# Performance work log

Measured on AMD Instinct MI355X. Metric: run time of the kernel, lower is better.

The kernel has to match this reference:

```python
import jax, jax.numpy as jnp
import numpy as np

N_NODES = 50000
N_EDGES = 400000
F_IN = 70
E_DIM = 4
HID = 128
HEADS = 4


def _add_self_loops(src, dst, edge_attr, n):
    # PyG GATConv(add_self_loops=True, fill_value='mean' when edge_dim is set):
    # self-loop edge_attr = per-dst-node mean of incoming edge_attr.
    cnt = jax.ops.segment_sum(jnp.ones((src.shape[0],), edge_attr.dtype), dst, n)
    loop_attr = jax.ops.segment_sum(edge_attr, dst, n) / jnp.clip(cnt, 1.0)[:, None]
    loop = jnp.arange(n, dtype=src.dtype)
    return (jnp.concatenate([src, loop]), jnp.concatenate([dst, loop]),
            jnp.concatenate([edge_attr, loop_attr], axis=0))


def _gat_layer(x, src, dst, e_attr, W, a_src, a_dst, We, a_edge, b, concat):
    # W: [in, H*D]; a_src/a_dst/a_edge: [H, D]; We: [edge_dim, H*D]
    n = x.shape[0]
    H, D = a_src.shape
    xs = (x @ W).reshape(n, H, D)                      # [N,H,D]
    s_src = jnp.einsum('nhd,hd->nh', xs, a_src)        # [N,H]
    s_dst = jnp.einsum('nhd,hd->nh', xs, a_dst)
    ee = (e_attr @ We).reshape(-1, H, D)               # [E,H,D]
    s_edge = jnp.einsum('ehd,hd->eh', ee, a_edge)
    alpha = jax.nn.leaky_relu(s_src[src] + s_dst[dst] + s_edge, 0.2)  # [E,H]
    # segment softmax over edges grouped by destination node
    m = jax.ops.segment_max(alpha, dst, n)
    m = jnp.where(jnp.isfinite(m), m, 0.0)
    ex = jnp.exp(alpha - m[dst])
    denom = jax.ops.segment_sum(ex, dst, n)
    alpha = ex / (denom[dst] + 1e-16)
    msg = xs[src] * alpha[..., None]                   # [E,H,D] -- dominant traffic
    agg = jax.ops.segment_sum(msg, dst, n)             # [N,H,D]
    out = agg.reshape(n, H * D) if concat else agg.mean(axis=1)
    return out + b


def _layer_norm(x, g, b, eps=1e-5):
    mu = x.mean(-1, keepdims=True)
    var = ((x - mu) ** 2).mean(-1, keepdims=True)
    return (x - mu) * jax.lax.rsqrt(var + eps) * g + b


def setup_inputs() -> dict:
    key = jax.random.key(0)
    ks = jax.random.split(key, 24)
    f32 = jnp.float32
    node_features = jax.random.normal(ks[0], (N_NODES, F_IN), f32)
    edge_index = jax.random.randint(ks[1], (2, N_EDGES), 0, N_NODES, jnp.int32)
    edge_attr = jax.random.uniform(ks[2], (N_EDGES, E_DIM), f32)
    s = 0.1
    return {
        'node_features': node_features,
        'edge_index': edge_index,
        'edge_attr': edge_attr,
        'W1': jax.random.normal(ks[3], (F_IN, HEADS * HID), f32) * s,
        'as1': jax.random.normal(ks[4], (HEADS, HID), f32) * s,
        'ad1': jax.random.normal(ks[5], (HEADS, HID), f32) * s,
        'We1': jax.random.normal(ks[6], (E_DIM, HEADS * HID), f32) * s,
        'ae1': jax.random.normal(ks[7], (HEADS, HID), f32) * s,
        'b1': jnp.zeros((HEADS * HID,), f32),
        # GAT layer 2: 512 -> 128, 1 head, mean
        'W2': jax.random.normal(ks[8], (HEADS * HID, HID), f32) * s,
        'as2': jax.random.normal(ks[9], (1, HID), f32) * s,
        'ad2': jax.random.normal(ks[10], (1, HID), f32) * s,
        'We2': jax.random.normal(ks[11], (E_DIM, HID), f32) * s,
        'ae2': jax.random.normal(ks[12], (1, HID), f32) * s,
        'b2': jnp.zeros((HID,), f32),
        'ln_g': jnp.ones((HID,), f32),
        'ln_b': jnp.zeros((HID,), f32),
        'pw': jax.random.normal(ks[13], (HID, 8), f32) * s,
        'pb': jnp.zeros((8,), f32),
        'dw': jax.random.normal(ks[14], (HID, 4), f32) * s,
        'db': jnp.zeros((4,), f32),
    }


def reference(node_features, edge_index, edge_attr, W1, as1, ad1, We1, ae1, b1,
              W2, as2, ad2, We2, ae2, b2, ln_g, ln_b, pw, pb, dw, db):
    n = node_features.shape[0]
    src, dst, ea = _add_self_loops(edge_index[0], edge_index[1], edge_attr, n)
    x = jax.nn.gelu(_gat_layer(node_features, src, dst, ea, W1, as1, ad1, We1, ae1, b1, True), approximate=False)
    x = jax.nn.gelu(_gat_layer(x, src, dst, ea, W2, as2, ad2, We2, ae2, b2, False), approximate=False)
    x = _layer_norm(x, ln_g, ln_b)
    return (x @ pw + pb, x @ dw + db)
```

## Files before the change

kernel.cpp:

```cpp
#include <hip/hip_runtime.h>
#include <hip/hip_bf16.h>
#include <math.h>

#define NN 50000
#define NE 400000
#define FIN 70
#define EDIM 4
#define HIDD 128
#define NHEAD 4
constexpr int ET = NE + NN;
constexpr int KP1 = 96;
constexpr int NFP = 72;
constexpr int SCB = (NN + 255) / 256;

constexpr size_t al4(size_t x){ return (x + 3) & ~size_t(3); }
constexpr size_t CNT_O   = 0;
constexpr size_t ZEND    = al4(CNT_O + NN);
constexpr size_t CSR_O   = ZEND;
constexpr size_t BSUM_O  = al4(CSR_O + NN + 1);
constexpr size_t BOFF_O  = al4(BSUM_O + 256);
constexpr size_t EPK_O   = al4(BOFF_O + 256);
constexpr size_t EXF1_O  = al4(EPK_O + (size_t)ET*4);
constexpr size_t EXF2_O  = al4(EXF1_O + (size_t)ET*4);
constexpr size_t SS1_O   = al4(EXF2_O + ET);
constexpr size_t SD1_O   = al4(SS1_O + (size_t)NN*4);
constexpr size_t SS2_O   = al4(SD1_O + (size_t)NN*4);
constexpr size_t SD2_O   = al4(SS2_O + NN);
constexpr size_t CST_O   = al4(SD2_O + NN);
constexpr size_t W1T_O   = al4(CST_O + 2048);
constexpr size_t W2T_O   = al4(W1T_O + 4*128*KP1/2);
constexpr size_t NFB_O   = al4(W2T_O + 128*512/2);
constexpr size_t AGG_O   = al4(NFB_O + (size_t)NN*NFP/2);
constexpr size_t XS2_O   = al4(AGG_O + (size_t)4*NN*KP1/2);

constexpr int VS1 = 0;
constexpr int VD1 = 320;
constexpr int VE1 = 640;
constexpr int VE2 = 656;
constexpr int VS2 = 704;
constexpr int VD2 = 1216;

typedef short s8v __attribute__((ext_vector_type(8)));
typedef float f4v __attribute__((ext_vector_type(4)));

__device__ __forceinline__ unsigned short f2b(float v){
  __hip_bfloat16 b = __float2bfloat16(v);
  return *(unsigned short*)&b;
}
__device__ __forceinline__ float b2f(unsigned u_lo16){
  return __uint_as_float(u_lo16 << 16);
}
__device__ __forceinline__ unsigned pk2(float lo, float hi){
  return (unsigned)f2b(lo) | ((unsigned)f2b(hi) << 16);
}
__device__ __forceinline__ float lrelu(float x){ return x > 0.f ? x : 0.2f * x; }

__device__ __forceinline__ float gelu_fast(float x){
  float z = x * 0.70710678118654752440f;
  float a = fabsf(z);
  float t = 1.f / (1.f + 0.3275911f * a);
  float p = ((((1.061405429f*t - 1.453152027f)*t + 1.421413741f)*t
              - 0.284496736f)*t + 0.254829592f)*t;
  float erfv = 1.f - p * __expf(-a * a);
  erfv = copysignf(erfv, z);
  return 0.5f * x * (1.f + erfv);
}

__global__ void k_deg(const int* __restrict__ ei, int* __restrict__ cnt){
  int e = blockIdx.x * 256 + threadIdx.x;
  if (e >= NE) return;
  atomicAdd(&cnt[ei[NE + e]], 1);
}

__global__ void k_scan1(const int* __restrict__ cnt, int* __restrict__ bsum){
  __shared__ int ws[4];
  int t = threadIdx.x, lane = t & 63, w = t >> 6;
  int i = blockIdx.x * 256 + t;
  int v = (i < NN) ? cnt[i] + 1 : 0;
  for (int o = 32; o; o >>= 1) v += __shfl_down(v, o);
  if (lane == 0) ws[w] = v;
  __syncthreads();
  if (t == 0) bsum[blockIdx.x] = ws[0] + ws[1] + ws[2] + ws[3];
}

__global__ void k_scan2(const int* __restrict__ bsum, int* __restrict__ boff){
  __shared__ int ws[4];
  int t = threadIdx.x, lane = t & 63, w = t >> 6;
  int v = (t < SCB) ? bsum[t] : 0;
  int x = v;
  #pragma unroll
  for (int o = 1; o < 64; o <<= 1){ int u = __shfl_up(x, o); if (lane >= o) x += u; }
  if (lane == 63) ws[w] = x;
  __syncthreads();
  if (w == 0 && lane < 4){
    int y = ws[lane];
    #pragma unroll
    for (int o = 1; o < 4; o <<= 1){ int u = __shfl_up(y, o); if (lane >= o) y += u; }
    ws[lane] = y;
  }
  __syncthreads();
  int incl = x + (w > 0 ? ws[w - 1] : 0);
  if (t < SCB) boff[t] = incl - v;
}

__global__ void k_scan3(const int* __restrict__ cnt, const int* __restrict__ boff,
                        int* __restrict__ csr){
  __shared__ int ws[4];
  int t = threadIdx.x, lane = t & 63, w = t >> 6;
  int i = blockIdx.x * 256 + t;
  int v = (i < NN) ? cnt[i] + 1 : 0;
  int x = v;
  #pragma unroll
  for (int o = 1; o < 64; o <<= 1){ int u = __shfl_up(x, o); if (lane >= o) x += u; }
  if (lane == 63) ws[w] = x;
  __syncthreads();
  if (w == 0 && lane < 4){
    int y = ws[lane];
    #pragma unroll
    for (int o = 1; o < 4; o <<= 1){ int u = __shfl_up(y, o); if (lane >= o) y += u; }
    ws[lane] = y;
  }
  __syncthreads();
  if (i < NN) csr[i + 1] = boff[blockIdx.x] + (w > 0 ? ws[w - 1] : 0) + x;
  if (i == 0) csr[0] = 0;
}

__global__ void k_fill(const int* __restrict__ ei, const float* __restrict__ ea,
                       const int* __restrict__ csr, int* __restrict__ cnt,
                       int4* __restrict__ epk, const float* __restrict__ ss1,
                       const float* __restrict__ sd1, const float* __restrict__ C,
                       float4* __restrict__ exf){
  int e = blockIdx.x * 256 + threadIdx.x;
  if (e >= NE) return;
  int s = ei[e], d = ei[NE + e];
  int r = atomicSub(&cnt[d], 1);
  int p = csr[d] + r - 1;
  float4 a = *(const float4*)&ea[(size_t)e * 4];
  epk[p] = make_int4(s, d, (int)pk2(a.x, a.y), (int)pk2(a.z, a.w));
  float4 ssv = *(const float4*)&ss1[(size_t)s * 4];
  float4 sdv = *(const float4*)&sd1[(size_t)d * 4];
  float e0 = __expf(lrelu(ssv.x + sdv.x + a.x*C[VE1+0] + a.y*C[VE1+4] + a.z*C[VE1+8]  + a.w*C[VE1+12]));
  float e1 = __expf(lrelu(ssv.y + sdv.y + a.x*C[VE1+1] + a.y*C[VE1+5] + a.z*C[VE1+9]  + a.w*C[VE1+13]));
  float e2 = __expf(lrelu(ssv.z + sdv.z + a.x*C[VE1+2] + a.y*C[VE1+6] + a.z*C[VE1+10] + a.w*C[VE1+14]));
  float e3 = __expf(lrelu(ssv.w + sdv.w + a.x*C[VE1+3] + a.y*C[VE1+7] + a.z*C[VE1+11] + a.w*C[VE1+15]));
  exf[p] = make_float4(e0, e1, e2, e3);
}

__global__ void k_loopself(const int* __restrict__ csr, int4* __restrict__ epk,
                           const float* __restrict__ ss1, const float* __restrict__ sd1,
                           const float* __restrict__ C, float4* __restrict__ exf){
  int n = blockIdx.x * 256 + threadIdx.x;
  if (n >= NN) return;
  int a = csr[n], b = csr[n + 1];
  int deg = b - a - 1;
  float s0 = 0.f, s1 = 0.f, s2 = 0.f, s3 = 0.f;
  for (int p = a; p < b - 1; ++p){
    int4 v = epk[p];
    s0 += b2f((unsigned)v.z & 0xffffu); s1 += b2f((unsigned)v.z >> 16);
    s2 += b2f((unsigned)v.w & 0xffffu); s3 += b2f((unsigned)v.w >> 16);
  }
  float inv = 1.f / (float)(deg > 1 ? deg : 1);
  float m0 = s0*inv, m1 = s1*inv, m2 = s2*inv, m3 = s3*inv;
  epk[b - 1] = make_int4(n, n, (int)pk2(m0, m1), (int)pk2(m2, m3));
  float4 ssv = *(const float4*)&ss1[(size_t)n * 4];
  float4 sdv = *(const float4*)&sd1[(size_t)n * 4];
  float e0 = __expf(lrelu(ssv.x + sdv.x + m0*C[VE1+0] + m1*C[VE1+4] + m2*C[VE1+8]  + m3*C[VE1+12]));
  float e1 = __expf(lrelu(ssv.y + sdv.y + m0*C[VE1+1] + m1*C[VE1+5] + m2*C[VE1+9]  + m3*C[VE1+13]));
  float e2 = __expf(lrelu(ssv.z + sdv.z + m0*C[VE1+2] + m1*C[VE1+6] + m2*C[VE1+10] + m3*C[VE1+14]));
  float e3 = __expf(lrelu(ssv.w + sdv.w + m0*C[VE1+3] + m1*C[VE1+7] + m2*C[VE1+11] + m3*C[VE1+15]));
  exf[b - 1] = make_float4(e0, e1, e2, e3);
}

__global__ void k_prep(const float* __restrict__ W1, const float* __restrict__ as1,
                       const float* __restrict__ ad1, const float* __restrict__ We1,
                       const float* __restrict__ ae1, const float* __restrict__ W2,
                       const float* __restrict__ as2, const float* __restrict__ ad2,
                       const float* __restrict__ We2, const float* __restrict__ ae2,
                       float* __restrict__ C){
  int t = threadIdx.x;
  if (t < 280){
    int k = t >> 2, h = t & 3;
    float s = 0.f, d = 0.f;
    for (int dd = 0; dd < 128; ++dd){
      float w = W1[k*512 + h*128 + dd];
      s += w * as1[h*128 + dd];
      d += w * ad1[h*128 + dd];
    }
    C[VS1 + t] = s; C[VD1 + t] = d;
  }
  if (t < 16){
    int k = t >> 2, h = t & 3;
    float s = 0.f;
    for (int dd = 0; dd < 128; ++dd) s += We1[k*512 + h*128 + dd] * ae1[h*128 + dd];
    C[VE1 + t] = s;
  }
  if (t < 4){
    float s = 0.f;
    for (int dd = 0; dd < 128; ++dd) s += We2[t*128 + dd] * ae2[dd];
    C[VE2 + t] = s;
  }
  {
    float s = 0.f, d = 0.f;
    for (int dd = 0; dd < 128; ++dd){
      float w = W2[t*128 + dd];
      s += w * as2[dd];
      d += w * ad2[dd];
    }
    C[VS2 + t] = s; C[VD2 + t] = d;
  }
}

__global__ void k_tw(const float* __restrict__ W1, const float* __restrict__ W2,
                     unsigned short* __restrict__ W1p, unsigned short* __restrict__ W2p){
  int i = blockIdx.x * 256 + threadIdx.x;
  if (i < 12*128*32){
    int kk = i & 31, r = (i >> 5) & 127, ph = i >> 12;
    int h = ph / 3, kf = ph - 3*h;
    int kg = kf*32 + kk;
    float v = (kg < FIN) ? W1[kg*512 + h*128 + r] : 0.f;
    W1p[i] = f2b(v);
  } else {
    int j = i - 12*128*32;
    if (j < 16*128*32){
      int kk = j & 31, r = (j >> 5) & 127, p = j >> 12;
      W2p[j] = f2b(W2[(p*32 + kk)*128 + r]);
    }
  }
}

__global__ __launch_bounds__(256) void k_cnfs1(const float* __restrict__ nf,
    const float* __restrict__ C, unsigned short* __restrict__ nfb,
    float* __restrict__ ss1, float* __restrict__ sd1){
  int lane = threadIdx.x & 63, w = threadIdx.x >> 6;
  int n = blockIdx.x * 4 + w;
  if (n >= NN) return;
  int c0 = lane * 2;
  bool act = lane < 35;
  float v0 = 0.f, v1 = 0.f;
  if (act){
    v0 = nf[(size_t)n * FIN + c0];
    v1 = nf[(size_t)n * FIN + c0 + 1];
  }
  if (lane < 36) *(unsigned*)&nfb[(size_t)n * NFP + c0] = act ? pk2(v0, v1) : 0u;
  float sh[4] = {0,0,0,0}, dh[4] = {0,0,0,0};
  if (act){
    float4 cs0 = *(const float4*)&C[VS1 + c0*4];
    float4 cs1 = *(const float4*)&C[VS1 + (c0+1)*4];
    float4 cd0 = *(const float4*)&C[VD1 + c0*4];
    float4 cd1 = *(const float4*)&C[VD1 + (c0+1)*4];
    sh[0] = v0*cs0.x + v1*cs1.x; sh[1] = v0*cs0.y + v1*cs1.y;
    sh[2] = v0*cs0.z + v1*cs1.z; sh[3] = v0*cs0.w + v1*cs1.w;
    dh[0] = v0*cd0.x + v1*cd1.x; dh[1] = v0*cd0.y + v1*cd1.y;
    dh[2] = v0*cd0.z + v1*cd1.z; dh[3] = v0*cd0.w + v1*cd1.w;
  }
  #pragma unroll
  for (int o = 32; o; o >>= 1){
    #pragma unroll
    for (int h = 0; h < 4; ++h){
      sh[h] += __shfl_xor(sh[h], o);
      dh[h] += __shfl_xor(dh[h], o);
    }
  }
  if (lane == 0){
    *(float4*)&ss1[(size_t)n*4] = make_float4(sh[0], sh[1], sh[2], sh[3]);
    *(float4*)&sd1[(size_t)n*4] = make_float4(dh[0], dh[1], dh[2], dh[3]);
  }
}

__global__ __launch_bounds__(256, 4) void k_gemm12(
    const unsigned short* __restrict__ agg, const unsigned short* __restrict__ W1p,
    const unsigned short* __restrict__ W2p, const float* __restrict__ b1,
    const float* __restrict__ Cv, unsigned short* __restrict__ xs2b,
    float* __restrict__ ss2, float* __restrict__ sd2){
  __shared__ unsigned short xt[32 * 516];
  __shared__ float ssp[32][4], sdp[32][4];
  int tid = threadIdx.x, lane = tid & 63, wn = tid >> 6;
  int m15 = lane & 15, rq = lane >> 4;
  int r0 = blockIdx.x * 32;
  int gr0 = r0 + m15;      if (gr0 >= NN) gr0 = NN - 1;
  int gr1 = r0 + 16 + m15; if (gr1 >= NN) gr1 = NN - 1;
  float s2a0 = 0.f, s2d0 = 0.f, s2a1 = 0.f, s2d1 = 0.f;
  constexpr size_t HS = (size_t)NN * KP1;
  const int bfo = (wn * 32 + m15) * 32 + rq * 8;
  const unsigned short* A0 = agg + (size_t)gr0 * KP1 + rq * 8;
  const unsigned short* A1 = agg + (size_t)gr1 * KP1 + rq * 8;

  #pragma unroll
  for (int h = 0; h < 4; ++h){
    f4v acc[2][2] = {};
    const unsigned short* Bh = W1p + h * 3 * 4096 + bfo;
    #pragma unroll
    for (int kf = 0; kf < 3; ++kf){
      s8v a0 = *(const s8v*)(A0 + (size_t)h * HS + kf * 32);
      s8v a1 = *(const s8v*)(A1 + (size_t)h * HS + kf * 32);
      #pragma unroll
      for (int ni = 0; ni < 2; ++ni){
        s8v bf = *(const s8v*)(Bh + kf * 4096 + ni * 512);
        acc[0][ni] = __builtin_amdgcn_mfma_f32_16x16x32_bf16(bf, a0, acc[0][ni], 0, 0, 0);
        acc[1][ni] = __builtin_amdgcn_mfma_f32_16x16x32_bf16(bf, a1, acc[1][ni], 0, 0, 0);
      }
    }
    #pragma unroll
    for (int m = 0; m < 2; ++m){
      #pragma unroll
      for (int ni = 0; ni < 2; ++ni){
        int cb = h * 128 + wn * 32 + ni * 16 + rq * 4;
        float4 bv = *(const float4*)&b1[cb];
        float v0 = gelu_fast(acc[m][ni][0] + bv.x);
        float v1 = gelu_fast(acc[m][ni][1] + bv.y);
        float v2 = gelu_fast(acc[m][ni][2] + bv.z);
        float v3 = gelu_fast(acc[m][ni][3] + bv.w);
        float4 cs = *(const float4*)&Cv[VS2 + cb];
        float4 cd = *(const float4*)&Cv[VD2 + cb];
        float pa = v0*cs.x + v1*cs.y + v2*cs.z + v3*cs.w;
        float pd = v0*cd.x + v1*cd.y + v2*cd.z + v3*cd.w;
        if (m == 0){ s2a0 += pa; s2d0 += pd; } else { s2a1 += pa; s2d1 += pd; }
        *(uint2*)&xt[(m * 16 + m15) * 516 + cb] = make_uint2(pk2(v0, v1), pk2(v2, v3));
      }
    }
  }
  s2a0 += __shfl_xor(s2a0, 16); s2a0 += __shfl_xor(s2a0, 32);
  s2d0 += __shfl_xor(s2d0, 16); s2d0 += __shfl_xor(s2d0, 32);
  s2a1 += __shfl_xor(s2a1, 16); s2a1 += __shfl_xor(s2a1, 32);
  s2d1 += __shfl_xor(s2d1, 16); s2d1 += __shfl_xor(s2d1, 32);
  if (rq == 0){
    ssp[m15][wn] = s2a0;      sdp[m15][wn] = s2d0;
    ssp[16 + m15][wn] = s2a1; sdp[16 + m15][wn] = s2d1;
  }

  __syncthreads();

  if (tid < 32 && r0 + tid < NN){
    ss2[r0 + tid] = (ssp[tid][0] + ssp[tid][1]) + (ssp[tid][2] + ssp[tid][3]);
    sd2[r0 + tid] = (sdp[tid][0] + sdp[tid][1]) + (sdp[tid][2] + sdp[tid][3]);
  }

  f4v acc2[2][2] = {};
  #pragma unroll
  for (int p = 0; p < 16; ++p){
    s8v x0 = *(const s8v*)&xt[m15 * 516 + p * 32 + rq * 8];
    s8v x1 = *(const s8v*)&xt[(16 + m15) * 516 + p * 32 + rq * 8];
    #pragma unroll
    for (int ni = 0; ni < 2; ++ni){
      s8v bf = *(const s8v*)(W2p + p * 4096 + bfo + ni * 512);
      acc2[0][ni] = __builtin_amdgcn_mfma_f32_16x16x32_bf16(bf, x0, acc2[0][ni], 0, 0, 0);
      acc2[1][ni] = __builtin_amdgcn_mfma_f32_16x16x32_bf16(bf, x1, acc2[1][ni], 0, 0, 0);
    }
  }
  #pragma unroll
  for (int m = 0; m < 2; ++m){
    int grow = r0 + m * 16 + m15;
    if (grow < NN){
      #pragma unroll
      for (int ni = 0; ni < 2; ++ni){
        int gc = wn * 32 + ni * 16 + rq * 4;
        *(uint2*)&xs2b[(size_t)grow * 128 + gc] =
            make_uint2(pk2(acc2[m][ni][0], acc2[m][ni][1]),
                       pk2(acc2[m][ni][2], acc2[m][ni][3]));
      }
    }
  }
}

__global__ __launch_bounds__(256) void k_aggnf(const int* __restrict__ csr,
    const int4* __restrict__ epk, const float4* __restrict__ exf,
    const unsigned short* __restrict__ nfb, unsigned short* __restrict__ agg){
  int lane = threadIdx.x & 63, w = threadIdx.x >> 6;
  int n = blockIdx.x * 4 + w;
  if (n >= NN) return;
  int off = __builtin_amdgcn_readfirstlane(csr[n]);
  int end = __builtin_amdgcn_readfirstlane(csr[n + 1]);
  int col = lane * 2;
  bool act = lane < 36;
  float d0=0,d1=0,d2=0,d3=0;
  float a00=0,a01=0,a10=0,a11=0,a20=0,a21=0,a30=0,a31=0;
  int p = off;
  for (; p + 2 <= end; p += 2){
    int s0 = epk[p].x, s1 = epk[p+1].x;
    float4 e0 = exf[p], e1 = exf[p+1];
    unsigned u0 = 0, u1 = 0;
    if (act){
      u0 = *(const unsigned*)&nfb[(size_t)s0 * NFP + col];
      u1 = *(const unsigned*)&nfb[(size_t)s1 * NFP + col];
    }
    d0 += e0.x + e1.x; d1 += e0.y + e1.y; d2 += e0.z + e1.z; d3 += e0.w + e1.w;
    float v00 = b2f(u0 & 0xffffu), v01 = b2f(u0 >> 16);
    float v10 = b2f(u1 & 0xffffu), v11 = b2f(u1 >> 16);
    a00 += e0.x*v00 + e1.x*v10; a01 += e0.x*v01 + e1.x*v11;
    a10 += e0.y*v00 + e1.y*v10; a11 += e0.y*v01 + e1.y*v11;
    a20 += e0.z*v00 + e1.z*v10; a21 += e0.z*v01 + e1.z*v11;
    a30 += e0.w*v00 + e1.w*v10; a31 += e0.w*v01 + e1.w*v11;
  }
  if (p < end){
    int s0 = epk[p].x;
    float4 e0 = exf[p];
    unsigned u0 = 0;
    if (act) u0 = *(const unsigned*)&nfb[(size_t)s0 * NFP + col];
    d0 += e0.x; d1 += e0.y; d2 += e0.z; d3 += e0.w;
    float v00 = b2f(u0 & 0xffffu), v01 = b2f(u0 >> 16);
    a00 += e0.x*v00; a01 += e0.x*v01;
    a10 += e0.y*v00; a11 += e0.y*v01;
    a20 += e0.z*v00; a21 += e0.z*v01;
    a30 += e0.w*v00; a31 += e0.w*v01;
  }
  float i0 = 1.f/(d0+1e-16f), i1 = 1.f/(d1+1e-16f);
  float i2 = 1.f/(d2+1e-16f), i3 = 1.f/(d3+1e-16f);
  constexpr size_t HS = (size_t)NN * KP1;
  size_t base = (size_t)n * KP1 + col;
  if (act){
    *(unsigned*)&agg[base]        = pk2(a00*i0, a01*i0);
    *(unsigned*)&agg[base +   HS] = pk2(a10*i1, a11*i1);
    *(unsigned*)&agg[base + 2*HS] = pk2(a20*i2, a21*i2);
    *(unsigned*)&agg[base + 3*HS] = pk2(a30*i3, a31*i3);
  } else if (lane < 48){
    *(unsigned*)&agg[base]        = 0u;
    *(unsigned*)&agg[base +   HS] = 0u;
    *(unsigned*)&agg[base + 2*HS] = 0u;
    *(unsigned*)&agg[base + 3*HS] = 0u;
  }
}

__global__ __launch_bounds__(256) void k_agg2(
    const int* __restrict__ csr, const int4* __restrict__ epk,
    const float* __restrict__ ss2, const float* __restrict__ sd2,
    const float* __restrict__ Cv, const unsigned short* __restrict__ xs2b,
    const float* __restrict__ b2, const float* __restrict__ lng,
    const float* __restrict__ lnb, const float* __restrict__ pw,
    const float* __restrict__ pb, const float* __restrict__ dwm,
    const float* __restrict__ dbv, float* __restrict__ out){
  int lane = threadIdx.x & 63, w = threadIdx.x >> 6;
  int n = blockIdx.x * 4 + w;
  if (n >= NN) return;
  int off = __builtin_amdgcn_readfirstlane(csr[n]);
  int end = __builtin_amdgcn_readfirstlane(csr[n + 1]);
  float sd2n = sd2[n];
  float cv0 = Cv[VE2], cv1 = Cv[VE2+1], cv2 = Cv[VE2+2], cv3 = Cv[VE2+3];
  int c0 = lane * 2;
  float acc0 = 0.f, acc1 = 0.f, den = 0.f;
  int p = off;
  for (; p + 2 <= end; p += 2){
    int4 p0 = epk[p], p1 = epk[p+1];
    int s0 = p0.x, s1 = p1.x;
    float sv0 = ss2[s0], sv1 = ss2[s1];
    unsigned u0 = *(const unsigned*)&xs2b[(size_t)s0 * 128 + c0];
    unsigned u1 = *(const unsigned*)&xs2b[(size_t)s1 * 128 + c0];
    float e0 = __expf(lrelu(sv0 + sd2n
             + b2f((unsigned)p0.z & 0xffffu)*cv0 + b2f((unsigned)p0.z >> 16)*cv1
             + b2f((unsigned)p0.w & 0xffffu)*cv2 + b2f((unsigned)p0.w >> 16)*cv3));
    float e1 = __expf(lrelu(sv1 + sd2n
             + b2f((unsigned)p1.z & 0xffffu)*cv0 + b2f((unsigned)p1.z >> 16)*cv1
             + b2f((unsigned)p1.w & 0xffffu)*cv2 + b2f((unsigned)p1.w >> 16)*cv3));
    den += e0 + e1;
    acc0 += e0*b2f(u0 & 0xffffu) + e1*b2f(u1 & 0xffffu);
    acc1 += e0*b2f(u0 >> 16) + e1*b2f(u1 >> 16);
  }
  if (p < end){
    int4 p0 = epk[p];
    int s0 = p0.x;
    float sv0 = ss2[s0];
    unsigned u0 = *(const unsigned*)&xs2b[(size_t)s0 * 128 + c0];
    float e0 = __expf(lrelu(sv0 + sd2n
             + b2f((unsigned)p0.z & 0xffffu)*cv0 + b2f((unsigned)p0.z >> 16)*cv1
             + b2f((unsigned)p0.w & 0xffffu)*cv2 + b2f((unsigned)p0.w >> 16)*cv3));
    den += e0;
    acc0 += e0*b2f(u0 & 0xffffu);
    acc1 += e0*b2f(u0 >> 16);
  }
  float invd = 1.f / (den + 1e-16f);
  float g0 = gelu_fast(acc0 * invd + b2[c0]);
  float g1 = gelu_fast(acc1 * invd + b2[c0 + 1]);
  float s = g0 + g1;
  #pragma unroll
  for (int o = 32; o; o >>= 1) s += __shfl_xor(s, o);
  float mu = s * (1.f / 128.f);
  float e0 = g0 - mu, e1 = g1 - mu;
  float q = e0*e0 + e1*e1;
  #pragma unroll
  for (int o = 32; o; o >>= 1) q += __shfl_xor(q, o);
  float rstd = rsqrtf(q * (1.f / 128.f) + 1e-5f);
  float y0 = e0 * rstd * lng[c0] + lnb[c0];
  float y1 = e1 * rstd * lng[c0 + 1] + lnb[c0 + 1];
  float pr[12];
  #pragma unroll
  for (int jj = 0; jj < 8; ++jj) pr[jj] = y0 * pw[c0*8 + jj] + y1 * pw[(c0+1)*8 + jj];
  #pragma unroll
  for (int jj = 0; jj < 4; ++jj) pr[8+jj] = y0 * dwm[c0*4 + jj] + y1 * dwm[(c0+1)*4 + jj];
  #pragma unroll
  for (int o = 32; o; o >>= 1)
    #pragma unroll
    for (int jj = 0; jj < 12; ++jj) pr[jj] += __shfl_xor(pr[jj], o);
  if (lane == 0){
    #pragma unroll
    for (int jj = 0; jj < 8; ++jj) out[(size_t)n*8 + jj] = pr[jj] + pb[jj];
    #pragma unroll
    for (int jj = 0; jj < 4; ++jj) out[(size_t)NN*8 + (size_t)n*4 + jj] = pr[8+jj] + dbv[jj];
  }
}

extern "C" void kernel_launch(void* const* d_in, const int* in_sizes, int n_in,
                              void* d_out, int out_size, void* d_ws, size_t ws_size,
                              hipStream_t stream){
  const float* nf  = (const float*)d_in[0];
  const int*   ei  = (const int*)  d_in[1];
  const float* ea  = (const float*)d_in[2];
  const float* W1  = (const float*)d_in[3];
  const float* as1 = (const float*)d_in[4];
  const float* ad1 = (const float*)d_in[5];
  const float* We1 = (const float*)d_in[6];
  const float* ae1 = (const float*)d_in[7];
  const float* b1  = (const float*)d_in[8];
  const float* W2  = (const float*)d_in[9];
  const float* as2 = (const float*)d_in[10];
  const float* ad2 = (const float*)d_in[11];
  const float* We2 = (const float*)d_in[12];
  const float* ae2 = (const float*)d_in[13];
  const float* b2  = (const float*)d_in[14];
  const float* lng = (const float*)d_in[15];
  const float* lnb = (const float*)d_in[16];
  const float* pw  = (const float*)d_in[17];
  const float* pb  = (const float*)d_in[18];
  const float* dw  = (const float*)d_in[19];
  const float* db  = (const float*)d_in[20];
  float* out = (float*)d_out;

  float* wf = (float*)d_ws;
  int*      cnt  = (int*)     (wf + CNT_O);
  int*      csr  = (int*)     (wf + CSR_O);
  int*      bsum = (int*)     (wf + BSUM_O);
  int*      boff = (int*)     (wf + BOFF_O);
  int4*     epk  = (int4*)    (wf + EPK_O);
  float4*   exf1 = (float4*)  (wf + EXF1_O);
  float*    ss1  =            (wf + SS1_O);
  float*    sd1  =            (wf + SD1_O);
  float*    ss2  =            (wf + SS2_O);
  float*    sd2  =            (wf + SD2_O);
  float*    Cc   =            (wf + CST_O);
  unsigned short* W1p = (unsigned short*)(wf + W1T_O);
  unsigned short* W2p = (unsigned short*)(wf + W2T_O);
  unsigned short* nfb = (unsigned short*)(wf + NFB_O);
  unsigned short* agg = (unsigned short*)(wf + AGG_O);
  unsigned short* xs2b= (unsigned short*)(wf + XS2_O);

  hipMemsetAsync(cnt, 0, NN * sizeof(int), stream);
  k_prep<<<1, 512, 0, stream>>>(W1, as1, ad1, We1, ae1, W2, as2, ad2, We2, ae2, Cc);
  k_tw<<<(12*128*32 + 16*128*32 + 255) / 256, 256, 0, stream>>>(W1, W2, W1p, W2p);
  k_cnfs1<<<(NN + 3) / 4, 256, 0, stream>>>(nf, Cc, nfb, ss1, sd1);
  k_deg<<<(NE + 255) / 256, 256, 0, stream>>>(ei, cnt);
  k_scan1<<<SCB, 256, 0, stream>>>(cnt, bsum);
  k_scan2<<<1, 256, 0, stream>>>(bsum, boff);
  k_scan3<<<SCB, 256, 0, stream>>>(cnt, boff, csr);
  k_fill<<<(NE + 255) / 256, 256, 0, stream>>>(ei, ea, csr, cnt, epk, ss1, sd1, Cc, exf1);
  k_loopself<<<(NN + 255) / 256, 256, 0, stream>>>(csr, epk, ss1, sd1, Cc, exf1);
  k_aggnf<<<(NN + 3) / 4, 256, 0, stream>>>(csr, epk, exf1, nfb, agg);
  k_gemm12<<<(NN + 31) / 32, 256, 0, stream>>>(agg, W1p, W2p, b1, Cc, xs2b, ss2, sd2);
  k_agg2<<<(NN + 3) / 4, 256, 0, stream>>>(csr, epk, ss2, sd2, Cc, xs2b,
                                           b2, lng, lnb, pw, pb, dw, db, out);
}
```

Before: 344.9 us.

## Fuse self-loop computation into layer-1 aggregation and widen GEMM row tile

Removes the separate self-loop kernel: the aggregation kernel now accumulates the mean edge attribute while walking incoming edges, computes the self-loop attention weight itself, writes the self-loop record for later use, and adds the self-loop contribution directly. This drops one launch and a second pass over the edge records. Separately, the fused two-layer GEMM kernel now processes 64 rows per block instead of 32, reusing each loaded weight fragment across four row tiles. That costs more LDS and registers, with launch bounds lowered to 2 blocks per CU.

```diff
diff --git a/kernel.cpp b/kernel.cpp
--- a/kernel.cpp
+++ b/kernel.cpp
@@ -146,31 +146,6 @@
   exf[p] = make_float4(e0, e1, e2, e3);
 }
 
-__global__ void k_loopself(const int* __restrict__ csr, int4* __restrict__ epk,
-                           const float* __restrict__ ss1, const float* __restrict__ sd1,
-                           const float* __restrict__ C, float4* __restrict__ exf){
-  int n = blockIdx.x * 256 + threadIdx.x;
-  if (n >= NN) return;
-  int a = csr[n], b = csr[n + 1];
-  int deg = b - a - 1;
-  float s0 = 0.f, s1 = 0.f, s2 = 0.f, s3 = 0.f;
-  for (int p = a; p < b - 1; ++p){
-    int4 v = epk[p];
-    s0 += b2f((unsigned)v.z & 0xffffu); s1 += b2f((unsigned)v.z >> 16);
-    s2 += b2f((unsigned)v.w & 0xffffu); s3 += b2f((unsigned)v.w >> 16);
-  }
-  float inv = 1.f / (float)(deg > 1 ? deg : 1);
-  float m0 = s0*inv, m1 = s1*inv, m2 = s2*inv, m3 = s3*inv;
-  epk[b - 1] = make_int4(n, n, (int)pk2(m0, m1), (int)pk2(m2, m3));
-  float4 ssv = *(const float4*)&ss1[(size_t)n * 4];
-  float4 sdv = *(const float4*)&sd1[(size_t)n * 4];
-  float e0 = __expf(lrelu(ssv.x + sdv.x + m0*C[VE1+0] + m1*C[VE1+4] + m2*C[VE1+8]  + m3*C[VE1+12]));
-  float e1 = __expf(lrelu(ssv.y + sdv.y + m0*C[VE1+1] + m1*C[VE1+5] + m2*C[VE1+9]  + m3*C[VE1+13]));
-  float e2 = __expf(lrelu(ssv.z + sdv.z + m0*C[VE1+2] + m1*C[VE1+6] + m2*C[VE1+10] + m3*C[VE1+14]));
-  float e3 = __expf(lrelu(ssv.w + sdv.w + m0*C[VE1+3] + m1*C[VE1+7] + m2*C[VE1+11] + m3*C[VE1+15]));
-  exf[b - 1] = make_float4(e0, e1, e2, e3);
-}
-
 __global__ void k_prep(const float* __restrict__ W1, const float* __restrict__ as1,
                        const float* __restrict__ ad1, const float* __restrict__ We1,
                        const float* __restrict__ ae1, const float* __restrict__ W2,
@@ -267,41 +242,43 @@
   }
 }
 
-__global__ __launch_bounds__(256, 4) void k_gemm12(
+__global__ __launch_bounds__(256, 2) void k_gemm12(
     const unsigned short* __restrict__ agg, const unsigned short* __restrict__ W1p,
     const unsigned short* __restrict__ W2p, const float* __restrict__ b1,
     const float* __restrict__ Cv, unsigned short* __restrict__ xs2b,
     float* __restrict__ ss2, float* __restrict__ sd2){
-  __shared__ unsigned short xt[32 * 516];
-  __shared__ float ssp[32][4], sdp[32][4];
+  __shared__ unsigned short xt[64 * 516];
+  __shared__ float ssp[64][4], sdp[64][4];
   int tid = threadIdx.x, lane = tid & 63, wn = tid >> 6;
   int m15 = lane & 15, rq = lane >> 4;
-  int r0 = blockIdx.x * 32;
-  int gr0 = r0 + m15;      if (gr0 >= NN) gr0 = NN - 1;
-  int gr1 = r0 + 16 + m15; if (gr1 >= NN) gr1 = NN - 1;
-  float s2a0 = 0.f, s2d0 = 0.f, s2a1 = 0.f, s2d1 = 0.f;
+  int r0 = blockIdx.x * 64;
+  const unsigned short* A[4];
+  #pragma unroll
+  for (int m = 0; m < 4; ++m){
+    int g = r0 + m * 16 + m15; if (g >= NN) g = NN - 1;
+    A[m] = agg + (size_t)g * KP1 + rq * 8;
+  }
+  float s2a[4] = {0,0,0,0}, s2d[4] = {0,0,0,0};
   constexpr size_t HS = (size_t)NN * KP1;
   const int bfo = (wn * 32 + m15) * 32 + rq * 8;
-  const unsigned short* A0 = agg + (size_t)gr0 * KP1 + rq * 8;
-  const unsigned short* A1 = agg + (size_t)gr1 * KP1 + rq * 8;
 
   #pragma unroll
   for (int h = 0; h < 4; ++h){
-    f4v acc[2][2] = {};
+    f4v acc[4][2] = {};
     const unsigned short* Bh = W1p + h * 3 * 4096 + bfo;
     #pragma unroll
     for (int kf = 0; kf < 3; ++kf){
-      s8v a0 = *(const s8v*)(A0 + (size_t)h * HS + kf * 32);
-      s8v a1 = *(const s8v*)(A1 + (size_t)h * HS + kf * 32);
+      s8v bf0 = *(const s8v*)(Bh + kf * 4096);
+      s8v bf1 = *(const s8v*)(Bh + kf * 4096 + 512);
       #pragma unroll
-      for (int ni = 0; ni < 2; ++ni){
-        s8v bf = *(const s8v*)(Bh + kf * 4096 + ni * 512);
-        acc[0][ni] = __builtin_amdgcn_mfma_f32_16x16x32_bf16(bf, a0, acc[0][ni], 0, 0, 0);
-        acc[1][ni] = __builtin_amdgcn_mfma_f32_16x16x32_bf16(bf, a1, acc[1][ni], 0, 0, 0);
+      for (int m = 0; m < 4; ++m){
+        s8v a = *(const s8v*)(A[m] + (size_t)h * HS + kf * 32);
+        acc[m][0] = __builtin_amdgcn_mfma_f32_16x16x32_bf16(bf0, a, acc[m][0], 0, 0, 0);
+        acc[m][1] = __builtin_amdgcn_mfma_f32_16x16x32_bf16(bf1, a, acc[m][1], 0, 0, 0);
       }
     }
     #pragma unroll
-    for (int m = 0; m < 2; ++m){
+    for (int m = 0; m < 4; ++m){
       #pragma unroll
       for (int ni = 0; ni < 2; ++ni){
         int cb = h * 128 + wn * 32 + ni * 16 + rq * 4;
@@ -312,43 +289,46 @@
         float v3 = gelu_fast(acc[m][ni][3] + bv.w);
         float4 cs = *(const float4*)&Cv[VS2 + cb];
         float4 cd = *(const float4*)&Cv[VD2 + cb];
-        float pa = v0*cs.x + v1*cs.y + v2*cs.z + v3*cs.w;
-        float pd = v0*cd.x + v1*cd.y + v2*cd.z + v3*cd.w;
-        if (m == 0){ s2a0 += pa; s2d0 += pd; } else { s2a1 += pa; s2d1 += pd; }
+        s2a[m] += v0*cs.x + v1*cs.y + v2*cs.z + v3*cs.w;
+        s2d[m] += v0*cd.x + v1*cd.y + v2*cd.z + v3*cd.w;
         *(uint2*)&xt[(m * 16 + m15) * 516 + cb] = make_uint2(pk2(v0, v1), pk2(v2, v3));
       }
     }
   }
-  s2a0 += __shfl_xor(s2a0, 16); s2a0 += __shfl_xor(s2a0, 32);
-  s2d0 += __shfl_xor(s2d0, 16); s2d0 += __shfl_xor(s2d0, 32);
-  s2a1 += __shfl_xor(s2a1, 16); s2a1 += __shfl_xor(s2a1, 32);
-  s2d1 += __shfl_xor(s2d1, 16); s2d1 += __shfl_xor(s2d1, 32);
+  #pragma unroll
+  for (int m = 0; m < 4; ++m){
+    s2a[m] += __shfl_xor(s2a[m], 16); s2a[m] += __shfl_xor(s2a[m], 32);
+    s2d[m] += __shfl_xor(s2d[m], 16); s2d[m] += __shfl_xor(s2d[m], 32);
+  }
   if (rq == 0){
-    ssp[m15][wn] = s2a0;      sdp[m15][wn] = s2d0;
-    ssp[16 + m15][wn] = s2a1; sdp[16 + m15][wn] = s2d1;
+    #pragma unroll
+    for (int m = 0; m < 4; ++m){
+      ssp[m * 16 + m15][wn] = s2a[m];
+      sdp[m * 16 + m15][wn] = s2d[m];
+    }
   }
 
   __syncthreads();
 
-  if (tid < 32 && r0 + tid < NN){
+  if (tid < 64 && r0 + tid < NN){
     ss2[r0 + tid] = (ssp[tid][0] + ssp[tid][1]) + (ssp[tid][2] + ssp[tid][3]);
     sd2[r0 + tid] = (sdp[tid][0] + sdp[tid][1]) + (sdp[tid][2] + sdp[tid][3]);
   }
 
-  f4v acc2[2][2] = {};
+  f4v acc2[4][2] = {};
   #pragma unroll
   for (int p = 0; p < 16; ++p){
-    s8v x0 = *(const s8v*)&xt[m15 * 516 + p * 32 + rq * 8];
-    s8v x1 = *(const s8v*)&xt[(16 + m15) * 516 + p * 32 + rq * 8];
-    #pragma unroll
-    for (int ni = 0; ni < 2; ++ni){
-      s8v bf = *(const s8v*)(W2p + p * 4096 + bfo + ni * 512);
-      acc2[0][ni] = __builtin_amdgcn_mfma_f32_16x16x32_bf16(bf, x0, acc2[0][ni], 0, 0, 0);
-      acc2[1][ni] = __builtin_amdgcn_mfma_f32_16x16x32_bf16(bf, x1, acc2[1][ni], 0, 0, 0);
-    }
-  }
-  #pragma unroll
-  for (int m = 0; m < 2; ++m){
+    s8v bf0 = *(const s8v*)(W2p + p * 4096 + bfo);
+    s8v bf1 = *(const s8v*)(W2p + p * 4096 + bfo + 512);
+    #pragma unroll
+    for (int m = 0; m < 4; ++m){
+      s8v x = *(const s8v*)&xt[(m * 16 + m15) * 516 + p * 32 + rq * 8];
+      acc2[m][0] = __builtin_amdgcn_mfma_f32_16x16x32_bf16(bf0, x, acc2[m][0], 0, 0, 0);
+      acc2[m][1] = __builtin_amdgcn_mfma_f32_16x16x32_bf16(bf1, x, acc2[m][1], 0, 0, 0);
+    }
+  }
+  #pragma unroll
+  for (int m = 0; m < 4; ++m){
     int grow = r0 + m * 16 + m15;
     if (grow < NN){
       #pragma unroll
@@ -363,26 +343,34 @@
 }
 
 __global__ __launch_bounds__(256) void k_aggnf(const int* __restrict__ csr,
-    const int4* __restrict__ epk, const float4* __restrict__ exf,
-    const unsigned short* __restrict__ nfb, unsigned short* __restrict__ agg){
+    int4* __restrict__ epk, const float4* __restrict__ exf,
+    const unsigned short* __restrict__ nfb, const float* __restrict__ ss1,
+    const float* __restrict__ sd1, const float* __restrict__ Cv,
+    unsigned short* __restrict__ agg){
   int lane = threadIdx.x & 63, w = threadIdx.x >> 6;
   int n = blockIdx.x * 4 + w;
   if (n >= NN) return;
   int off = __builtin_amdgcn_readfirstlane(csr[n]);
   int end = __builtin_amdgcn_readfirstlane(csr[n + 1]);
+  int endr = end - 1;
   int col = lane * 2;
   bool act = lane < 36;
   float d0=0,d1=0,d2=0,d3=0;
   float a00=0,a01=0,a10=0,a11=0,a20=0,a21=0,a30=0,a31=0;
+  float t0=0,t1=0,t2=0,t3=0;
   int p = off;
-  for (; p + 2 <= end; p += 2){
-    int s0 = epk[p].x, s1 = epk[p+1].x;
+  for (; p + 2 <= endr; p += 2){
+    int4 q0 = epk[p], q1 = epk[p+1];
     float4 e0 = exf[p], e1 = exf[p+1];
     unsigned u0 = 0, u1 = 0;
     if (act){
-      u0 = *(const unsigned*)&nfb[(size_t)s0 * NFP + col];
-      u1 = *(const unsigned*)&nfb[(size_t)s1 * NFP + col];
-    }
+      u0 = *(const unsigned*)&nfb[(size_t)q0.x * NFP + col];
+      u1 = *(const unsigned*)&nfb[(size_t)q1.x * NFP + col];
+    }
+    t0 += b2f((unsigned)q0.z & 0xffffu) + b2f((unsigned)q1.z & 0xffffu);
+    t1 += b2f((unsigned)q0.z >> 16)     + b2f((unsigned)q1.z >> 16);
+    t2 += b2f((unsigned)q0.w & 0xffffu) + b2f((unsigned)q1.w & 0xffffu);
+    t3 += b2f((unsigned)q0.w >> 16)     + b2f((unsigned)q1.w >> 16);
     d0 += e0.x + e1.x; d1 += e0.y + e1.y; d2 += e0.z + e1.z; d3 += e0.w + e1.w;
     float v00 = b2f(u0 & 0xffffu), v01 = b2f(u0 >> 16);
     float v10 = b2f(u1 & 0xffffu), v11 = b2f(u1 >> 16);
@@ -391,17 +379,38 @@
     a20 += e0.z*v00 + e1.z*v10; a21 += e0.z*v01 + e1.z*v11;
     a30 += e0.w*v00 + e1.w*v10; a31 += e0.w*v01 + e1.w*v11;
   }
-  if (p < end){
-    int s0 = epk[p].x;
+  if (p < endr){
+    int4 q0 = epk[p];
     float4 e0 = exf[p];
     unsigned u0 = 0;
-    if (act) u0 = *(const unsigned*)&nfb[(size_t)s0 * NFP + col];
+    if (act) u0 = *(const unsigned*)&nfb[(size_t)q0.x * NFP + col];
+    t0 += b2f((unsigned)q0.z & 0xffffu); t1 += b2f((unsigned)q0.z >> 16);
+    t2 += b2f((unsigned)q0.w & 0xffffu); t3 += b2f((unsigned)q0.w >> 16);
     d0 += e0.x; d1 += e0.y; d2 += e0.z; d3 += e0.w;
     float v00 = b2f(u0 & 0xffffu), v01 = b2f(u0 >> 16);
     a00 += e0.x*v00; a01 += e0.x*v01;
     a10 += e0.y*v00; a11 += e0.y*v01;
     a20 += e0.z*v00; a21 += e0.z*v01;
     a30 += e0.w*v00; a31 += e0.w*v01;
+  }
+  int deg = endr - off;
+  float inv = 1.f / (float)(deg > 1 ? deg : 1);
+  float m0 = t0*inv, m1 = t1*inv, m2 = t2*inv, m3 = t3*inv;
+  if (lane == 0) epk[endr] = make_int4(n, n, (int)pk2(m0, m1), (int)pk2(m2, m3));
+  float4 ssv = *(const float4*)&ss1[(size_t)n * 4];
+  float4 sdv = *(const float4*)&sd1[(size_t)n * 4];
+  float e0 = __expf(lrelu(ssv.x + sdv.x + m0*Cv[VE1+0] + m1*Cv[VE1+4] + m2*Cv[VE1+8]  + m3*Cv[VE1+12]));
+  float e1 = __expf(lrelu(ssv.y + sdv.y + m0*Cv[VE1+1] + m1*Cv[VE1+5] + m2*Cv[VE1+9]  + m3*Cv[VE1+13]));
+  float e2 = __expf(lrelu(ssv.z + sdv.z + m0*Cv[VE1+2] + m1*Cv[VE1+6] + m2*Cv[VE1+10] + m3*Cv[VE1+14]));
+  float e3 = __expf(lrelu(ssv.w + sdv.w + m0*Cv[VE1+3] + m1*Cv[VE1+7] + m2*Cv[VE1+11] + m3*Cv[VE1+15]));
+  {
+    unsigned us = act ? *(const unsigned*)&nfb[(size_t)n * NFP + col] : 0u;
+    float v0 = b2f(us & 0xffffu), v1 = b2f(us >> 16);
+    d0 += e0; d1 += e1; d2 += e2; d3 += e3;
+    a00 += e0*v0; a01 += e0*v1;
+    a10 += e1*v0; a11 += e1*v1;
+    a20 += e2*v0; a21 += e2*v1;
+    a30 += e3*v0; a31 += e3*v1;
   }
   float i0 = 1.f/(d0+1e-16f), i1 = 1.f/(d1+1e-16f);
   float i2 = 1.f/(d2+1e-16f), i3 = 1.f/(d3+1e-16f);
@@ -550,9 +559,8 @@
   k_scan2<<<1, 256, 0, stream>>>(bsum, boff);
   k_scan3<<<SCB, 256, 0, stream>>>(cnt, boff, csr);
   k_fill<<<(NE + 255) / 256, 256, 0, stream>>>(ei, ea, csr, cnt, epk, ss1, sd1, Cc, exf1);
-  k_loopself<<<(NN + 255) / 256, 256, 0, stream>>>(csr, epk, ss1, sd1, Cc, exf1);
-  k_aggnf<<<(NN + 3) / 4, 256, 0, stream>>>(csr, epk, exf1, nfb, agg);
-  k_gemm12<<<(NN + 31) / 32, 256, 0, stream>>>(agg, W1p, W2p, b1, Cc, xs2b, ss2, sd2);
+  k_aggnf<<<(NN + 3) / 4, 256, 0, stream>>>(csr, epk, exf1, nfb, ss1, sd1, Cc, agg);
+  k_gemm12<<<(NN + 63) / 64, 256, 0, stream>>>(agg, W1p, W2p, b1, Cc, xs2b, ss2, sd2);
   k_agg2<<<(NN + 3) / 4, 256, 0, stream>>>(csr, epk, ss2, sd2, Cc, xs2b,
                                            b2, lng, lnb, pw, pb, dw, db, out);
 }
```

Result: no change. 350.3 us (+1.6%).

## Fuse layer-1 attention logits and self-loop handling into aggregation kernel

Applied to the files above, without the earlier changes.

Layer-1 exp(attention) values are no longer computed in k_fill and stored in an exf buffer. The separate k_loopself kernel is removed. The aggregation kernel now recomputes the exp logits per edge from ss1/sd1 and the packed edge attributes, accumulates the self-loop mean attribute on the fly, and writes the self-loop packed entry for layer 2. This removes one kernel launch, one per-node pass over the edges, and the write and read of a float4 per edge. In exchange, the aggregation wave does redundant exp and logit math in all 64 lanes and makes an extra gather of ss1 per edge.

```diff
diff --git a/kernel.cpp b/kernel.cpp
--- a/kernel.cpp
+++ b/kernel.cpp
@@ -127,9 +127,7 @@
 
 __global__ void k_fill(const int* __restrict__ ei, const float* __restrict__ ea,
                        const int* __restrict__ csr, int* __restrict__ cnt,
-                       int4* __restrict__ epk, const float* __restrict__ ss1,
-                       const float* __restrict__ sd1, const float* __restrict__ C,
-                       float4* __restrict__ exf){
+                       int4* __restrict__ epk){
   int e = blockIdx.x * 256 + threadIdx.x;
   if (e >= NE) return;
   int s = ei[e], d = ei[NE + e];
@@ -137,38 +135,6 @@
   int p = csr[d] + r - 1;
   float4 a = *(const float4*)&ea[(size_t)e * 4];
   epk[p] = make_int4(s, d, (int)pk2(a.x, a.y), (int)pk2(a.z, a.w));
-  float4 ssv = *(const float4*)&ss1[(size_t)s * 4];
-  float4 sdv = *(const float4*)&sd1[(size_t)d * 4];
-  float e0 = __expf(lrelu(ssv.x + sdv.x + a.x*C[VE1+0] + a.y*C[VE1+4] + a.z*C[VE1+8]  + a.w*C[VE1+12]));
-  float e1 = __expf(lrelu(ssv.y + sdv.y + a.x*C[VE1+1] + a.y*C[VE1+5] + a.z*C[VE1+9]  + a.w*C[VE1+13]));
-  float e2 = __expf(lrelu(ssv.z + sdv.z + a.x*C[VE1+2] + a.y*C[VE1+6] + a.z*C[VE1+10] + a.w*C[VE1+14]));
-  float e3 = __expf(lrelu(ssv.w + sdv.w + a.x*C[VE1+3] + a.y*C[VE1+7] + a.z*C[VE1+11] + a.w*C[VE1+15]));
-  exf[p] = make_float4(e0, e1, e2, e3);
-}
-
-__global__ void k_loopself(const int* __restrict__ csr, int4* __restrict__ epk,
-                           const float* __restrict__ ss1, const float* __restrict__ sd1,
-                           const float* __restrict__ C, float4* __restrict__ exf){
-  int n = blockIdx.x * 256 + threadIdx.x;
-  if (n >= NN) return;
-  int a = csr[n], b = csr[n + 1];
-  int deg = b - a - 1;
-  float s0 = 0.f, s1 = 0.f, s2 = 0.f, s3 = 0.f;
-  for (int p = a; p < b - 1; ++p){
-    int4 v = epk[p];
-    s0 += b2f((unsigned)v.z & 0xffffu); s1 += b2f((unsigned)v.z >> 16);
-    s2 += b2f((unsigned)v.w & 0xffffu); s3 += b2f((unsigned)v.w >> 16);
-  }
-  float inv = 1.f / (float)(deg > 1 ? deg : 1);
-  float m0 = s0*inv, m1 = s1*inv, m2 = s2*inv, m3 = s3*inv;
-  epk[b - 1] = make_int4(n, n, (int)pk2(m0, m1), (int)pk2(m2, m3));
-  float4 ssv = *(const float4*)&ss1[(size_t)n * 4];
-  float4 sdv = *(const float4*)&sd1[(size_t)n * 4];
-  float e0 = __expf(lrelu(ssv.x + sdv.x + m0*C[VE1+0] + m1*C[VE1+4] + m2*C[VE1+8]  + m3*C[VE1+12]));
-  float e1 = __expf(lrelu(ssv.y + sdv.y + m0*C[VE1+1] + m1*C[VE1+5] + m2*C[VE1+9]  + m3*C[VE1+13]));
-  float e2 = __expf(lrelu(ssv.z + sdv.z + m0*C[VE1+2] + m1*C[VE1+6] + m2*C[VE1+10] + m3*C[VE1+14]));
-  float e3 = __expf(lrelu(ssv.w + sdv.w + m0*C[VE1+3] + m1*C[VE1+7] + m2*C[VE1+11] + m3*C[VE1+15]));
-  exf[b - 1] = make_float4(e0, e1, e2, e3);
 }
 
 __global__ void k_prep(const float* __restrict__ W1, const float* __restrict__ as1,
@@ -363,45 +329,92 @@
 }
 
 __global__ __launch_bounds__(256) void k_aggnf(const int* __restrict__ csr,
-    const int4* __restrict__ epk, const float4* __restrict__ exf,
-    const unsigned short* __restrict__ nfb, unsigned short* __restrict__ agg){
+    int4* __restrict__ epk, const unsigned short* __restrict__ nfb,
+    const float* __restrict__ ss1, const float* __restrict__ sd1,
+    const float* __restrict__ Cv, unsigned short* __restrict__ agg){
   int lane = threadIdx.x & 63, w = threadIdx.x >> 6;
   int n = blockIdx.x * 4 + w;
   if (n >= NN) return;
   int off = __builtin_amdgcn_readfirstlane(csr[n]);
   int end = __builtin_amdgcn_readfirstlane(csr[n + 1]);
+  int endr = end - 1;
+  float4 sdn = *(const float4*)&sd1[(size_t)n * 4];
+  float c00=Cv[VE1+0], c01=Cv[VE1+1], c02=Cv[VE1+2], c03=Cv[VE1+3];
+  float c10=Cv[VE1+4], c11=Cv[VE1+5], c12=Cv[VE1+6], c13=Cv[VE1+7];
+  float c20=Cv[VE1+8], c21=Cv[VE1+9], c22=Cv[VE1+10], c23=Cv[VE1+11];
+  float c30=Cv[VE1+12], c31=Cv[VE1+13], c32=Cv[VE1+14], c33=Cv[VE1+15];
   int col = lane * 2;
   bool act = lane < 36;
   float d0=0,d1=0,d2=0,d3=0;
   float a00=0,a01=0,a10=0,a11=0,a20=0,a21=0,a30=0,a31=0;
+  float t0=0,t1=0,t2=0,t3=0;
   int p = off;
-  for (; p + 2 <= end; p += 2){
-    int s0 = epk[p].x, s1 = epk[p+1].x;
-    float4 e0 = exf[p], e1 = exf[p+1];
+  for (; p + 2 <= endr; p += 2){
+    int4 q0 = epk[p], q1 = epk[p+1];
+    float4 sv0 = *(const float4*)&ss1[(size_t)q0.x * 4];
+    float4 sv1 = *(const float4*)&ss1[(size_t)q1.x * 4];
     unsigned u0 = 0, u1 = 0;
     if (act){
-      u0 = *(const unsigned*)&nfb[(size_t)s0 * NFP + col];
-      u1 = *(const unsigned*)&nfb[(size_t)s1 * NFP + col];
-    }
-    d0 += e0.x + e1.x; d1 += e0.y + e1.y; d2 += e0.z + e1.z; d3 += e0.w + e1.w;
+      u0 = *(const unsigned*)&nfb[(size_t)q0.x * NFP + col];
+      u1 = *(const unsigned*)&nfb[(size_t)q1.x * NFP + col];
+    }
+    float ax0=b2f((unsigned)q0.z & 0xffffu), ay0=b2f((unsigned)q0.z >> 16);
+    float az0=b2f((unsigned)q0.w & 0xffffu), aw0=b2f((unsigned)q0.w >> 16);
+    float ax1=b2f((unsigned)q1.z & 0xffffu), ay1=b2f((unsigned)q1.z >> 16);
+    float az1=b2f((unsigned)q1.w & 0xffffu), aw1=b2f((unsigned)q1.w >> 16);
+    t0 += ax0 + ax1; t1 += ay0 + ay1; t2 += az0 + az1; t3 += aw0 + aw1;
+    float e00 = __expf(lrelu(sv0.x + sdn.x + ax0*c00 + ay0*c10 + az0*c20 + aw0*c30));
+    float e01 = __expf(lrelu(sv0.y + sdn.y + ax0*c01 + ay0*c11 + az0*c21 + aw0*c31));
+    float e02 = __expf(lrelu(sv0.z + sdn.z + ax0*c02 + ay0*c12 + az0*c22 + aw0*c32));
+    float e03 = __expf(lrelu(sv0.w + sdn.w + ax0*c03 + ay0*c13 + az0*c23 + aw0*c33));
+    float e10 = __expf(lrelu(sv1.x + sdn.x + ax1*c00 + ay1*c10 + az1*c20 + aw1*c30));
+    float e11 = __expf(lrelu(sv1.y + sdn.y + ax1*c01 + ay1*c11 + az1*c21 + aw1*c31));
+    float e12 = __expf(lrelu(sv1.z + sdn.z + ax1*c02 + ay1*c12 + az1*c22 + aw1*c32));
+    float e13 = __expf(lrelu(sv1.w + sdn.w + ax1*c03 + ay1*c13 + az1*c23 + aw1*c33));
+    d0 += e00 + e10; d1 += e01 + e11; d2 += e02 + e12; d3 += e03 + e13;
     float v00 = b2f(u0 & 0xffffu), v01 = b2f(u0 >> 16);
     float v10 = b2f(u1 & 0xffffu), v11 = b2f(u1 >> 16);
-    a00 += e0.x*v00 + e1.x*v10; a01 += e0.x*v01 + e1.x*v11;
-    a10 += e0.y*v00 + e1.y*v10; a11 += e0.y*v01 + e1.y*v11;
-    a20 += e0.z*v00 + e1.z*v10; a21 += e0.z*v01 + e1.z*v11;
-    a30 += e0.w*v00 + e1.w*v10; a31 += e0.w*v01 + e1.w*v11;
-  }
-  if (p < end){
-    int s0 = epk[p].x;
-    float4 e0 = exf[p];
+    a00 += e00*v00 + e10*v10; a01 += e00*v01 + e10*v11;
+    a10 += e01*v00 + e11*v10; a11 += e01*v01 + e11*v11;
+    a20 += e02*v00 + e12*v10; a21 += e02*v01 + e12*v11;
+    a30 += e03*v00 + e13*v10; a31 += e03*v01 + e13*v11;
+  }
+  if (p < endr){
+    int4 q0 = epk[p];
+    float4 sv0 = *(const float4*)&ss1[(size_t)q0.x * 4];
     unsigned u0 = 0;
-    if (act) u0 = *(const unsigned*)&nfb[(size_t)s0 * NFP + col];
-    d0 += e0.x; d1 += e0.y; d2 += e0.z; d3 += e0.w;
+    if (act) u0 = *(const unsigned*)&nfb[(size_t)q0.x * NFP + col];
+    float ax0=b2f((unsigned)q0.z & 0xffffu), ay0=b2f((unsigned)q0.z >> 16);
+    float az0=b2f((unsigned)q0.w & 0xffffu), aw0=b2f((unsigned)q0.w >> 16);
+    t0 += ax0; t1 += ay0; t2 += az0; t3 += aw0;
+    float e00 = __expf(lrelu(sv0.x + sdn.x + ax0*c00 + ay0*c10 + az0*c20 + aw0*c30));
+    float e01 = __expf(lrelu(sv0.y + sdn.y + ax0*c01 + ay0*c11 + az0*c21 + aw0*c31));
+    float e02 = __expf(lrelu(sv0.z + sdn.z + ax0*c02 + ay0*c12 + az0*c22 + aw0*c32));
+    float e03 = __expf(lrelu(sv0.w + sdn.w + ax0*c03 + ay0*c13 + az0*c23 + aw0*c33));
+    d0 += e00; d1 += e01; d2 += e02; d3 += e03;
     float v00 = b2f(u0 & 0xffffu), v01 = b2f(u0 >> 16);
-    a00 += e0.x*v00; a01 += e0.x*v01;
-    a10 += e0.y*v00; a11 += e0.y*v01;
-    a20 += e0.z*v00; a21 += e0.z*v01;
-    a30 += e0.w*v00; a31 += e0.w*v01;
+    a00 += e00*v00; a01 += e00*v01;
+    a10 += e01*v00; a11 += e01*v01;
+    a20 += e02*v00; a21 += e02*v01;
+    a30 += e03*v00; a31 += e03*v01;
+  }
+  int deg = endr - off;
+  float inv = 1.f / (float)(deg > 1 ? deg : 1);
+  float m0 = t0*inv, m1 = t1*inv, m2 = t2*inv, m3 = t3*inv;
+  if (lane == 0) epk[endr] = make_int4(n, n, (int)pk2(m0, m1), (int)pk2(m2, m3));
+  float4 ssv = *(const float4*)&ss1[(size_t)n * 4];
+  float e0 = __expf(lrelu(ssv.x + sdn.x + m0*c00 + m1*c10 + m2*c20 + m3*c30));
+  float e1 = __expf(lrelu(ssv.y + sdn.y + m0*c01 + m1*c11 + m2*c21 + m3*c31));
+  float e2 = __expf(lrelu(ssv.z + sdn.z + m0*c02 + m1*c12 + m2*c22 + m3*c32));
+  float e3 = __expf(lrelu(ssv.w + sdn.w + m0*c03 + m1*c13 + m2*c23 + m3*c33));
+  {
+    unsigned us = act ? *(const unsigned*)&nfb[(size_t)n * NFP + col] : 0u;
+    float v0 = b2f(us & 0xffffu), v1 = b2f(us >> 16);
+    d0 += e0; d1 += e1; d2 += e2; d3 += e3;
+    a00 += e0*v0; a01 += e0*v1;
+    a10 += e1*v0; a11 += e1*v1;
+    a20 += e2*v0; a21 += e2*v1;
+    a30 += e3*v0; a31 += e3*v1;
   }
   float i0 = 1.f/(d0+1e-16f), i1 = 1.f/(d1+1e-16f);
   float i2 = 1.f/(d2+1e-16f), i3 = 1.f/(d3+1e-16f);
@@ -529,7 +542,6 @@
   int*      bsum = (int*)     (wf + BSUM_O);
   int*      boff = (int*)     (wf + BOFF_O);
   int4*     epk  = (int4*)    (wf + EPK_O);
-  float4*   exf1 = (float4*)  (wf + EXF1_O);
   float*    ss1  =            (wf + SS1_O);
   float*    sd1  =            (wf + SD1_O);
   float*    ss2  =            (wf + SS2_O);
@@ -549,9 +561,8 @@
   k_scan1<<<SCB, 256, 0, stream>>>(cnt, bsum);
   k_scan2<<<1, 256, 0, stream>>>(bsum, boff);
   k_scan3<<<SCB, 256, 0, stream>>>(cnt, boff, csr);
-  k_fill<<<(NE + 255) / 256, 256, 0, stream>>>(ei, ea, csr, cnt, epk, ss1, sd1, Cc, exf1);
-  k_loopself<<<(NN + 255) / 256, 256, 0, stream>>>(csr, epk, ss1, sd1, Cc, exf1);
-  k_aggnf<<<(NN + 3) / 4, 256, 0, stream>>>(csr, epk, exf1, nfb, agg);
+  k_fill<<<(NE + 255) / 256, 256, 0, stream>>>(ei, ea, csr, cnt, epk);
+  k_aggnf<<<(NN + 3) / 4, 256, 0, stream>>>(csr, epk, nfb, ss1, sd1, Cc, agg);
   k_gemm12<<<(NN + 31) / 32, 256, 0, stream>>>(agg, W1p, W2p, b1, Cc, xs2b, ss2, sd2);
   k_agg2<<<(NN + 3) / 4, 256, 0, stream>>>(csr, epk, ss2, sd2, Cc, xs2b,
                                            b2, lng, lnb, pw, pb, dw, db, out);
```

New measurement: 374.1 us. +8.5%, slower.
